# Kernel optimization log

Hardware: AMD Instinct MI355X
Metric: run time of the kernel (lower is better)

## Reference

```python
import jax, jax.numpy as jnp
import numpy as np

DIM = 128
HEADS = 4
WH, WW = 7, 7
N = WH * WW
NW = 256   # windows per image (mask groups)
B = 64     # batch images
B_ = NW * B


def _relative_position_index():
    coords = np.stack(np.meshgrid(np.arange(WH), np.arange(WW), indexing='ij'))  # [2,Wh,Ww]
    cf = coords.reshape(2, -1)
    rel = cf[:, :, None] - cf[:, None, :]          # [2,N,N]
    rel = rel.transpose(1, 2, 0).copy()
    rel[:, :, 0] += WH - 1
    rel[:, :, 1] += WW - 1
    rel[:, :, 0] *= 2 * WW - 1
    return rel.sum(-1).astype(np.int32)            # [N,N]


def setup_inputs() -> dict:
    key = jax.random.key(0)
    ks = jax.random.split(key, 8)
    std = 0.02
    return {
        'x': jax.random.normal(ks[0], (B_, N, DIM), jnp.float32),
        'mask': jax.random.normal(ks[1], (NW, N, N), jnp.float32),
        'qkv_w': jax.random.normal(ks[2], (3 * DIM, DIM), jnp.float32) * std,
        'qkv_b': jnp.zeros((3 * DIM,), jnp.float32),
        'proj_w': jax.random.normal(ks[3], (DIM, DIM), jnp.float32) * std,
        'proj_b': jnp.zeros((DIM,), jnp.float32),
        'rpb_table': jax.random.normal(ks[4], ((2 * WH - 1) * (2 * WW - 1), HEADS), jnp.float32) * std,
        'rpi': jnp.asarray(_relative_position_index()),
    }


def reference(x, mask, qkv_w, qkv_b, proj_w, proj_b, rpb_table, rpi):
    head_dim = DIM // HEADS
    scale = head_dim ** -0.5
    # qkv projection: [B_, N, 3*C] -> [3, B_, H, N, hd]
    qkv = (jnp.einsum('bnc,dc->bnd', x, qkv_w) + qkv_b)
    qkv = qkv.reshape(B_, N, 3, HEADS, head_dim).transpose(2, 0, 3, 1, 4)
    q, k, v = qkv[0] * scale, qkv[1], qkv[2]
    attn = jnp.einsum('bhnd,bhmd->bhnm', q, k)       # [B_, H, N, N]
    # gathered relative position bias: [N,N,H] -> [H,N,N]
    bias = rpb_table[rpi.reshape(-1)].reshape(N, N, HEADS).transpose(2, 0, 1)
    attn = attn + bias[None]
    # additive window mask: group B_ into (B, NW)
    attn = attn.reshape(B_ // NW, NW, HEADS, N, N) + mask[None, :, None]
    attn = attn.reshape(B_, HEADS, N, N)
    attn = jax.nn.softmax(attn, axis=-1)
    out = jnp.einsum('bhnm,bhmd->bnhd', attn, v).reshape(B_, N, DIM)
    out = jnp.einsum('bnc,dc->bnd', out, proj_w) + proj_b
    return out
```

## Files before the change

### kernel.cpp

```cpp
#include <hip/hip_runtime.h>

typedef __attribute__((ext_vector_type(8))) short sh8;
typedef __attribute__((ext_vector_type(4))) float f32x4;

#define MFMA(a, b, c) __builtin_amdgcn_mfma_f32_16x16x32_bf16(a, b, c, 0, 0, 0)

__device__ __forceinline__ short f2bf(float f) {
    unsigned u = __builtin_bit_cast(unsigned, f);
    u += 0x7fffu + ((u >> 16) & 1u);
    return (short)(u >> 16);
}

#define B_   16384
#define NW   256
#define NT   49
#define DIM  128
#define HEADS 4
#define HD   32
#define SCALE 0.17677669529663687f

#define V_BYTES     205520896u
#define AMASK_OFF   205520896u
#define QW_OFF      222298112u
#define PW_OFF      222396416u

__global__ __launch_bounds__(256) void wa_prep(
    const float* __restrict__ mask, const float* __restrict__ rpb,
    const int* __restrict__ rpi, const float* __restrict__ qkv_w,
    const float* __restrict__ proj_w, float* __restrict__ amask,
    short* __restrict__ qw, short* __restrict__ pw) {
    int g = blockIdx.x * 256 + threadIdx.x;
    int c = g & 63, r = (g >> 6) & 63, wi = (g >> 12) & 255, h = g >> 20;
    float v;
    if (c < NT) {
        v = 0.f;
        if (r < NT) {
            int idx = r * NT + c;
            v = rpb[rpi[idx] * HEADS + h] + mask[wi * (NT * NT) + idx];
        }
    } else {
        v = -1e30f;
    }
    amask[g] = v;
    if (g < 384 * 128) qw[g] = f2bf(qkv_w[g]);
    if (g < 128 * 128) pw[g] = f2bf(proj_w[g]);
}

__global__ __launch_bounds__(256, 2) void wa_qkv(
    const float* __restrict__ x, const short* __restrict__ qw,
    const float* __restrict__ qkv_b, short* __restrict__ qk,
    short* __restrict__ vbuf) {
    __shared__ short lA[128 * 152];
    __shared__ short lB[128 * 152];
    const int tid = threadIdx.x;
    const int bid = blockIdx.x;
    const int sel = bid % 3;
    const int bm  = bid / 3;

    {
        const float* xb = x + (size_t)bm * 128 * 128;
#pragma unroll
        for (int i = 0; i < 8; i++) {
            int chunk = i * 256 + tid;
            int row = chunk >> 4, col = (chunk & 15) * 8;
            float4 v0 = *(const float4*)(xb + row * 128 + col);
            float4 v1 = *(const float4*)(xb + row * 128 + col + 4);
            sh8 o;
            o[0] = f2bf(v0.x); o[1] = f2bf(v0.y); o[2] = f2bf(v0.z); o[3] = f2bf(v0.w);
            o[4] = f2bf(v1.x); o[5] = f2bf(v1.y); o[6] = f2bf(v1.z); o[7] = f2bf(v1.w);
            *(sh8*)(&lA[row * 152 + col]) = o;
        }
        const short* wb = qw + sel * 128 * 128;
#pragma unroll
        for (int i = 0; i < 8; i++) {
            int chunk = i * 256 + tid;
            int row = chunk >> 4, col = (chunk & 15) * 8;
            *(sh8*)(&lB[row * 152 + col]) = *(const sh8*)(wb + row * 128 + col);
        }
    }
    __syncthreads();

    const int lane = tid & 63, wid = tid >> 6;
    const int quad = lane >> 4, l15 = lane & 15;
    const int wm = (wid & 1) * 64, wn = (wid >> 1) * 64;

    f32x4 acc[4][4] = {};
#pragma unroll
    for (int ks = 0; ks < 4; ks++) {
        sh8 a[4], b[4];
#pragma unroll
        for (int t = 0; t < 4; t++)
            a[t] = *(const sh8*)(&lA[(wm + t * 16 + l15) * 152 + ks * 32 + quad * 8]);
#pragma unroll
        for (int t = 0; t < 4; t++)
            b[t] = *(const sh8*)(&lB[(wn + t * 16 + l15) * 152 + ks * 32 + quad * 8]);
#pragma unroll
        for (int ti = 0; ti < 4; ti++)
#pragma unroll
            for (int tj = 0; tj < 4; tj++)
                acc[ti][tj] = MFMA(a[ti], b[tj], acc[ti][tj]);
    }

    float bv[4]; int hh[4], ee[4];
#pragma unroll
    for (int tj = 0; tj < 4; tj++) {
        int n = wn + tj * 16 + l15;
        bv[tj] = qkv_b[sel * 128 + n];
        hh[tj] = n >> 5; ee[tj] = n & 31;
    }
    short* outp = (sel < 2) ? qk : vbuf;
#pragma unroll
    for (int ti = 0; ti < 4; ti++)
#pragma unroll
        for (int reg = 0; reg < 4; reg++) {
            int t = bm * 128 + wm + ti * 16 + quad * 4 + reg;
            unsigned bwin = (unsigned)t / 49u;
            int nn = t - bwin * 49u;
#pragma unroll
            for (int tj = 0; tj < 4; tj++) {
                float v = acc[ti][tj][reg] + bv[tj];
                if (sel == 0) v *= SCALE;
                size_t dst;
                if (sel < 2)
                    dst = (size_t)bwin * 12544 + (size_t)sel * 6272 +
                          (size_t)(hh[tj] * NT + nn) * HD + ee[tj];
                else
                    dst = (((size_t)bwin * HEADS + hh[tj]) * NT + nn) * HD + ee[tj];
                outp[dst] = f2bf(v);
            }
        }
}

__global__ __launch_bounds__(256, 2) void wa_attn(
    const short* __restrict__ qk, const short* __restrict__ vbuf,
    const float* __restrict__ amask, const short* __restrict__ pw,
    const float* __restrict__ proj_b, float* __restrict__ out) {
    __shared__ short smem[33792];
    const int tid = threadIdx.x, lane = tid & 63, wid = tid >> 6;
    const int quad = lane >> 4, l15 = lane & 15;
    const int b = blockIdx.x, wi = b & 255;
    short* Pl = smem + wid * 5632;
    short* Vl = smem + 22528 + wid * 2816;

    {
        const short* vb = vbuf + ((size_t)b * HEADS + wid) * NT * HD;
#pragma unroll
        for (int i = 0; i < 4; i++) {
            int chunk = i * 64 + lane;
            int token = chunk >> 2, colc = (chunk & 3) * 8;
            sh8 v = (sh8)(short)0;
            if (token < NT) v = *(const sh8*)(vb + token * HD + colc);
#pragma unroll
            for (int j = 0; j < 8; j++) Vl[(colc + j) * 88 + token] = v[j];
        }
    }

    const short* qb = qk + (size_t)b * 12544 + wid * NT * HD;
    const short* kb = qb + 6272;
    sh8 aq[4], bk[4];
#pragma unroll
    for (int t = 0; t < 4; t++) {
        int tok = t * 16 + l15;
        sh8 z = (sh8)(short)0;
        aq[t] = z; bk[t] = z;
        if (tok < NT) {
            aq[t] = *(const sh8*)(qb + tok * HD + quad * 8);
            bk[t] = *(const sh8*)(kb + tok * HD + quad * 8);
        }
    }
    f32x4 S[4][4] = {};
#pragma unroll
    for (int ti = 0; ti < 4; ti++)
#pragma unroll
        for (int tj = 0; tj < 4; tj++) S[ti][tj] = MFMA(aq[ti], bk[tj], S[ti][tj]);

    const float* am = amask + (((size_t)wid * NW + wi) << 12);
    float rinv[4][4];
#pragma unroll
    for (int ti = 0; ti < 4; ti++)
#pragma unroll
        for (int reg = 0; reg < 4; reg++) {
            int row = ti * 16 + quad * 4 + reg;
            float mx = -1e38f;
#pragma unroll
            for (int tj = 0; tj < 4; tj++) {
                float lg = S[ti][tj][reg] + am[row * 64 + tj * 16 + l15];
                S[ti][tj][reg] = lg;
                mx = fmaxf(mx, lg);
            }
#pragma unroll
            for (int d = 1; d < 16; d <<= 1) mx = fmaxf(mx, __shfl_xor(mx, d, 64));
            float sum = 0.f;
#pragma unroll
            for (int tj = 0; tj < 4; tj++) {
                float p = __expf(S[ti][tj][reg] - mx);
                S[ti][tj][reg] = p;
                sum += p;
            }
#pragma unroll
            for (int d = 1; d < 16; d <<= 1) sum += __shfl_xor(sum, d, 64);
            rinv[ti][reg] = 1.f / sum;
        }

#pragma unroll
    for (int ti = 0; ti < 4; ti++)
#pragma unroll
        for (int reg = 0; reg < 4; reg++) {
            int row = ti * 16 + quad * 4 + reg;
#pragma unroll
            for (int tj = 0; tj < 4; tj++)
                Pl[row * 88 + tj * 16 + l15] = f2bf(S[ti][tj][reg]);
        }

    f32x4 CV[4][2] = {};
#pragma unroll
    for (int ks = 0; ks < 2; ks++) {
        sh8 pa[4], vv[2];
#pragma unroll
        for (int t = 0; t < 4; t++)
            pa[t] = *(const sh8*)(&Pl[(t * 16 + l15) * 88 + ks * 32 + quad * 8]);
#pragma unroll
        for (int t = 0; t < 2; t++)
            vv[t] = *(const sh8*)(&Vl[(t * 16 + l15) * 88 + ks * 32 + quad * 8]);
#pragma unroll
        for (int ti = 0; ti < 4; ti++)
#pragma unroll
            for (int tj = 0; tj < 2; tj++) CV[ti][tj] = MFMA(pa[ti], vv[tj], CV[ti][tj]);
    }

    __syncthreads();

#pragma unroll
    for (int ti = 0; ti < 4; ti++)
#pragma unroll
        for (int reg = 0; reg < 4; reg++) {
            int row = ti * 16 + quad * 4 + reg;
            float inv = rinv[ti][reg];
#pragma unroll
            for (int tj = 0; tj < 2; tj++)
                smem[row * 152 + wid * 32 + tj * 16 + l15] = f2bf(CV[ti][tj][reg] * inv);
        }
    __syncthreads();

    f32x4 O[4][2] = {};
    const short* pwb = pw + (wid * 32) * 128;
#pragma unroll
    for (int ks = 0; ks < 4; ks++) {
        sh8 ca[4], wb2[2];
#pragma unroll
        for (int t = 0; t < 4; t++)
            ca[t] = *(const sh8*)(&smem[(t * 16 + l15) * 152 + ks * 32 + quad * 8]);
#pragma unroll
        for (int t = 0; t < 2; t++)
            wb2[t] = *(const sh8*)(pwb + (t * 16 + l15) * 128 + ks * 32 + quad * 8);
#pragma unroll
        for (int ti = 0; ti < 4; ti++)
#pragma unroll
            for (int tj = 0; tj < 2; tj++) O[ti][tj] = MFMA(ca[ti], wb2[tj], O[ti][tj]);
    }
    float pb[2];
#pragma unroll
    for (int t = 0; t < 2; t++) pb[t] = proj_b[wid * 32 + t * 16 + l15];
    float* ob = out + (size_t)b * NT * DIM;
#pragma unroll
    for (int ti = 0; ti < 4; ti++)
#pragma unroll
        for (int reg = 0; reg < 4; reg++) {
            int row = ti * 16 + quad * 4 + reg;
            if (row < NT) {
#pragma unroll
                for (int tj = 0; tj < 2; tj++)
                    ob[row * DIM + wid * 32 + tj * 16 + l15] = O[ti][tj][reg] + pb[tj];
            }
        }
}

extern "C" void kernel_launch(void* const* d_in, const int* in_sizes, int n_in,
                              void* d_out, int out_size, void* d_ws, size_t ws_size,
                              hipStream_t stream) {
    const float* x      = (const float*)d_in[0];
    const float* mask   = (const float*)d_in[1];
    const float* qkv_w  = (const float*)d_in[2];
    const float* qkv_b  = (const float*)d_in[3];
    const float* proj_w = (const float*)d_in[4];
    const float* proj_b = (const float*)d_in[5];
    const float* rpb    = (const float*)d_in[6];
    const int*   rpi    = (const int*)d_in[7];

    char* ws = (char*)d_ws;
    short* vbuf  = (short*)ws;
    float* amask = (float*)(ws + AMASK_OFF);
    short* qw    = (short*)(ws + QW_OFF);
    short* pw    = (short*)(ws + PW_OFF);
    short* qkbuf = (short*)d_out;
    float* out   = (float*)d_out;

    wa_prep<<<16384, 256, 0, stream>>>(mask, rpb, rpi, qkv_w, proj_w, amask, qw, pw);
    wa_qkv<<<6272 * 3, 256, 0, stream>>>(x, qw, qkv_b, qkbuf, vbuf);
    wa_attn<<<B_, 256, 0, stream>>>(qkbuf, vbuf, amask, pw, proj_b, out);
}
```

Before: 1.246 ms.

## Reuse converted x tile across Q/K/V, transpose scores, and swizzle LDS

The QKV kernel now converts each x tile to bf16 once and loops over the three weight slices, reading weights straight from global memory instead of staging them in LDS. This removes the threefold x reads and conversions and halves LDS use, which allows higher occupancy. The attention kernel computes S transposed so each lane holds a query row's keys, letting it use vectorized float4 mask loads and cut the row reductions to two shuffles. It also normalizes P before writing it, packs bf16 with v_cvt_pk_bf16_f32, and uses XOR-swizzled LDS layouts in place of padded ones, shrinking shared memory. The risks are extra latency from global weight loads and possible bank conflicts from the swizzle pattern.

```diff
diff --git a/kernel.cpp b/kernel.cpp
--- a/kernel.cpp
+++ b/kernel.cpp
@@ -9,6 +9,11 @@
     unsigned u = __builtin_bit_cast(unsigned, f);
     u += 0x7fffu + ((u >> 16) & 1u);
     return (short)(u >> 16);
+}
+__device__ __forceinline__ unsigned pk_bf16(float lo, float hi) {
+    unsigned r;
+    asm("v_cvt_pk_bf16_f32 %0, %1, %2" : "=v"(r) : "v"(lo), "v"(hi));
+    return r;
 }
 
 #define B_   16384
@@ -46,36 +51,25 @@
     if (g < 128 * 128) pw[g] = f2bf(proj_w[g]);
 }
 
-__global__ __launch_bounds__(256, 2) void wa_qkv(
+__global__ __launch_bounds__(256, 4) void wa_qkv(
     const float* __restrict__ x, const short* __restrict__ qw,
     const float* __restrict__ qkv_b, short* __restrict__ qk,
     short* __restrict__ vbuf) {
     __shared__ short lA[128 * 152];
-    __shared__ short lB[128 * 152];
     const int tid = threadIdx.x;
-    const int bid = blockIdx.x;
-    const int sel = bid % 3;
-    const int bm  = bid / 3;
-
+    const int bm = blockIdx.x;
     {
-        const float* xb = x + (size_t)bm * 128 * 128;
+        const float* xb = x + (size_t)bm * (128 * 128);
 #pragma unroll
         for (int i = 0; i < 8; i++) {
             int chunk = i * 256 + tid;
             int row = chunk >> 4, col = (chunk & 15) * 8;
             float4 v0 = *(const float4*)(xb + row * 128 + col);
             float4 v1 = *(const float4*)(xb + row * 128 + col + 4);
-            sh8 o;
-            o[0] = f2bf(v0.x); o[1] = f2bf(v0.y); o[2] = f2bf(v0.z); o[3] = f2bf(v0.w);
-            o[4] = f2bf(v1.x); o[5] = f2bf(v1.y); o[6] = f2bf(v1.z); o[7] = f2bf(v1.w);
-            *(sh8*)(&lA[row * 152 + col]) = o;
-        }
-        const short* wb = qw + sel * 128 * 128;
-#pragma unroll
-        for (int i = 0; i < 8; i++) {
-            int chunk = i * 256 + tid;
-            int row = chunk >> 4, col = (chunk & 15) * 8;
-            *(sh8*)(&lB[row * 152 + col]) = *(const sh8*)(wb + row * 128 + col);
+            uint4 u;
+            u.x = pk_bf16(v0.x, v0.y); u.y = pk_bf16(v0.z, v0.w);
+            u.z = pk_bf16(v1.x, v1.y); u.w = pk_bf16(v1.z, v1.w);
+            *(uint4*)(&lA[row * 152 + col]) = u;
         }
     }
     __syncthreads();
@@ -84,66 +78,70 @@
     const int quad = lane >> 4, l15 = lane & 15;
     const int wm = (wid & 1) * 64, wn = (wid >> 1) * 64;
 
-    f32x4 acc[4][4] = {};
-#pragma unroll
-    for (int ks = 0; ks < 4; ks++) {
-        sh8 a[4], b[4];
-#pragma unroll
-        for (int t = 0; t < 4; t++)
-            a[t] = *(const sh8*)(&lA[(wm + t * 16 + l15) * 152 + ks * 32 + quad * 8]);
-#pragma unroll
-        for (int t = 0; t < 4; t++)
-            b[t] = *(const sh8*)(&lB[(wn + t * 16 + l15) * 152 + ks * 32 + quad * 8]);
-#pragma unroll
-        for (int ti = 0; ti < 4; ti++)
-#pragma unroll
-            for (int tj = 0; tj < 4; tj++)
-                acc[ti][tj] = MFMA(a[ti], b[tj], acc[ti][tj]);
-    }
-
-    float bv[4]; int hh[4], ee[4];
-#pragma unroll
-    for (int tj = 0; tj < 4; tj++) {
-        int n = wn + tj * 16 + l15;
-        bv[tj] = qkv_b[sel * 128 + n];
-        hh[tj] = n >> 5; ee[tj] = n & 31;
-    }
-    short* outp = (sel < 2) ? qk : vbuf;
-#pragma unroll
-    for (int ti = 0; ti < 4; ti++)
-#pragma unroll
-        for (int reg = 0; reg < 4; reg++) {
-            int t = bm * 128 + wm + ti * 16 + quad * 4 + reg;
-            unsigned bwin = (unsigned)t / 49u;
-            int nn = t - bwin * 49u;
-#pragma unroll
-            for (int tj = 0; tj < 4; tj++) {
-                float v = acc[ti][tj][reg] + bv[tj];
-                if (sel == 0) v *= SCALE;
-                size_t dst;
-                if (sel < 2)
-                    dst = (size_t)bwin * 12544 + (size_t)sel * 6272 +
-                          (size_t)(hh[tj] * NT + nn) * HD + ee[tj];
-                else
-                    dst = (((size_t)bwin * HEADS + hh[tj]) * NT + nn) * HD + ee[tj];
-                outp[dst] = f2bf(v);
+#pragma unroll 1
+    for (int sel = 0; sel < 3; sel++) {
+        const short* wb = qw + sel * (128 * 128);
+        f32x4 acc[4][4] = {};
+#pragma unroll
+        for (int ks = 0; ks < 4; ks++) {
+            sh8 a[4], b[4];
+#pragma unroll
+            for (int t = 0; t < 4; t++)
+                a[t] = *(const sh8*)(&lA[(wm + t * 16 + l15) * 152 + ks * 32 + quad * 8]);
+#pragma unroll
+            for (int t = 0; t < 4; t++)
+                b[t] = *(const sh8*)(wb + (wn + t * 16 + l15) * 128 + ks * 32 + quad * 8);
+#pragma unroll
+            for (int ti = 0; ti < 4; ti++)
+#pragma unroll
+                for (int tj = 0; tj < 4; tj++)
+                    acc[ti][tj] = MFMA(a[ti], b[tj], acc[ti][tj]);
+        }
+        float bv[4]; int hh[4], ee[4];
+#pragma unroll
+        for (int tj = 0; tj < 4; tj++) {
+            int n = wn + tj * 16 + l15;
+            bv[tj] = qkv_b[sel * 128 + n];
+            hh[tj] = n >> 5; ee[tj] = n & 31;
+        }
+        short* outp = (sel < 2) ? qk : vbuf;
+#pragma unroll
+        for (int ti = 0; ti < 4; ti++)
+#pragma unroll
+            for (int reg = 0; reg < 4; reg++) {
+                int t = bm * 128 + wm + ti * 16 + quad * 4 + reg;
+                unsigned bwin = (unsigned)t / 49u;
+                int nn = t - bwin * 49u;
+#pragma unroll
+                for (int tj = 0; tj < 4; tj++) {
+                    float v = acc[ti][tj][reg] + bv[tj];
+                    if (sel == 0) v *= SCALE;
+                    size_t dst;
+                    if (sel < 2)
+                        dst = (size_t)bwin * 12544 + (size_t)sel * 6272 +
+                              (size_t)(hh[tj] * NT + nn) * HD + ee[tj];
+                    else
+                        dst = (((size_t)bwin * HEADS + hh[tj]) * NT + nn) * HD + ee[tj];
+                    outp[dst] = f2bf(v);
+                }
             }
-        }
-}
-
-__global__ __launch_bounds__(256, 2) void wa_attn(
+    }
+}
+
+__global__ __launch_bounds__(256, 3) void wa_attn(
     const short* __restrict__ qk, const short* __restrict__ vbuf,
     const float* __restrict__ amask, const short* __restrict__ pw,
     const float* __restrict__ proj_b, float* __restrict__ out) {
-    __shared__ short smem[33792];
+    __shared__ short smem[24576];
     const int tid = threadIdx.x, lane = tid & 63, wid = tid >> 6;
     const int quad = lane >> 4, l15 = lane & 15;
     const int b = blockIdx.x, wi = b & 255;
-    short* Pl = smem + wid * 5632;
-    short* Vl = smem + 22528 + wid * 2816;
+    short* Pl = smem + wid * 4096;
+    short* Vl = smem + 16384 + wid * 2048;
+    const int swz = (l15 & 7) << 3;
 
     {
-        const short* vb = vbuf + ((size_t)b * HEADS + wid) * NT * HD;
+        const short* vb = vbuf + ((size_t)b * HEADS + wid) * (NT * HD);
 #pragma unroll
         for (int i = 0; i < 4; i++) {
             int chunk = i * 64 + lane;
@@ -151,11 +149,12 @@
             sh8 v = (sh8)(short)0;
             if (token < NT) v = *(const sh8*)(vb + token * HD + colc);
 #pragma unroll
-            for (int j = 0; j < 8; j++) Vl[(colc + j) * 88 + token] = v[j];
-        }
-    }
-
-    const short* qb = qk + (size_t)b * 12544 + wid * NT * HD;
+            for (int j = 0; j < 8; j++)
+                Vl[(colc + j) * 64 + (token ^ (j << 3))] = v[j];
+        }
+    }
+
+    const short* qb = qk + (size_t)b * 12544 + wid * (NT * HD);
     const short* kb = qb + 6272;
     sh8 aq[4], bk[4];
 #pragma unroll
@@ -172,73 +171,72 @@
 #pragma unroll
     for (int ti = 0; ti < 4; ti++)
 #pragma unroll
-        for (int tj = 0; tj < 4; tj++) S[ti][tj] = MFMA(aq[ti], bk[tj], S[ti][tj]);
+        for (int tj = 0; tj < 4; tj++) S[ti][tj] = MFMA(bk[ti], aq[tj], S[ti][tj]);
 
     const float* am = amask + (((size_t)wid * NW + wi) << 12);
-    float rinv[4][4];
+#pragma unroll
+    for (int tj = 0; tj < 4; tj++) {
+        const int q = tj * 16 + l15;
+        float mx = -1e38f;
+#pragma unroll
+        for (int ti = 0; ti < 4; ti++) {
+            float4 m4 = *(const float4*)(am + q * 64 + ti * 16 + quad * 4);
+            S[ti][tj][0] += m4.x; S[ti][tj][1] += m4.y;
+            S[ti][tj][2] += m4.z; S[ti][tj][3] += m4.w;
+#pragma unroll
+            for (int r = 0; r < 4; r++) mx = fmaxf(mx, S[ti][tj][r]);
+        }
+        mx = fmaxf(mx, __shfl_xor(mx, 16));
+        mx = fmaxf(mx, __shfl_xor(mx, 32));
+        float sum = 0.f;
+#pragma unroll
+        for (int ti = 0; ti < 4; ti++)
+#pragma unroll
+            for (int r = 0; r < 4; r++) {
+                float p = __expf(S[ti][tj][r] - mx);
+                S[ti][tj][r] = p;
+                sum += p;
+            }
+        sum += __shfl_xor(sum, 16);
+        sum += __shfl_xor(sum, 32);
+        float inv = 1.f / sum;
+        short* pq = Pl + q * 64;
+#pragma unroll
+        for (int ti = 0; ti < 4; ti++) {
+            uint2 u;
+            u.x = pk_bf16(S[ti][tj][0] * inv, S[ti][tj][1] * inv);
+            u.y = pk_bf16(S[ti][tj][2] * inv, S[ti][tj][3] * inv);
+            *(uint2*)(pq + ((ti * 16 + quad * 4) ^ swz)) = u;
+        }
+    }
+
+    f32x4 CV[4][2] = {};
+#pragma unroll
+    for (int ks = 0; ks < 2; ks++) {
+        sh8 pa[4], vv[2];
+#pragma unroll
+        for (int t = 0; t < 4; t++)
+            pa[t] = *(const sh8*)(Pl + (t * 16 + l15) * 64 + ((ks * 32 + quad * 8) ^ swz));
+#pragma unroll
+        for (int t = 0; t < 2; t++)
+            vv[t] = *(const sh8*)(Vl + (t * 16 + l15) * 64 + ((ks * 32 + quad * 8) ^ swz));
+#pragma unroll
+        for (int ti = 0; ti < 4; ti++)
+#pragma unroll
+            for (int tj = 0; tj < 2; tj++) CV[ti][tj] = MFMA(pa[ti], vv[tj], CV[ti][tj]);
+    }
+
+    __syncthreads();
+
 #pragma unroll
     for (int ti = 0; ti < 4; ti++)
 #pragma unroll
         for (int reg = 0; reg < 4; reg++) {
             int row = ti * 16 + quad * 4 + reg;
-            float mx = -1e38f;
-#pragma unroll
-            for (int tj = 0; tj < 4; tj++) {
-                float lg = S[ti][tj][reg] + am[row * 64 + tj * 16 + l15];
-                S[ti][tj][reg] = lg;
-                mx = fmaxf(mx, lg);
-            }
-#pragma unroll
-            for (int d = 1; d < 16; d <<= 1) mx = fmaxf(mx, __shfl_xor(mx, d, 64));
-            float sum = 0.f;
-#pragma unroll
-            for (int tj = 0; tj < 4; tj++) {
-                float p = __expf(S[ti][tj][reg] - mx);
-                S[ti][tj][reg] = p;
-                sum += p;
-            }
-#pragma unroll
-            for (int d = 1; d < 16; d <<= 1) sum += __shfl_xor(sum, d, 64);
-            rinv[ti][reg] = 1.f / sum;
-        }
-
-#pragma unroll
-    for (int ti = 0; ti < 4; ti++)
-#pragma unroll
-        for (int reg = 0; reg < 4; reg++) {
-            int row = ti * 16 + quad * 4 + reg;
-#pragma unroll
-            for (int tj = 0; tj < 4; tj++)
-                Pl[row * 88 + tj * 16 + l15] = f2bf(S[ti][tj][reg]);
-        }
-
-    f32x4 CV[4][2] = {};
-#pragma unroll
-    for (int ks = 0; ks < 2; ks++) {
-        sh8 pa[4], vv[2];
-#pragma unroll
-        for (int t = 0; t < 4; t++)
-            pa[t] = *(const sh8*)(&Pl[(t * 16 + l15) * 88 + ks * 32 + quad * 8]);
-#pragma unroll
-        for (int t = 0; t < 2; t++)
-            vv[t] = *(const sh8*)(&Vl[(t * 16 + l15) * 88 + ks * 32 + quad * 8]);
-#pragma unroll
-        for (int ti = 0; ti < 4; ti++)
-#pragma unroll
-            for (int tj = 0; tj < 2; tj++) CV[ti][tj] = MFMA(pa[ti], vv[tj], CV[ti][tj]);
-    }
-
-    __syncthreads();
-
-#pragma unroll
-    for (int ti = 0; ti < 4; ti++)
-#pragma unroll
-        for (int reg = 0; reg < 4; reg++) {
-            int row = ti * 16 + quad * 4 + reg;
-            float inv = rinv[ti][reg];
+            int rs = (row & 7) << 3;
 #pragma unroll
             for (int tj = 0; tj < 2; tj++)
-                smem[row * 152 + wid * 32 + tj * 16 + l15] = f2bf(CV[ti][tj][reg] * inv);
+                smem[row * 128 + ((wid * 32 + tj * 16 + l15) ^ rs)] = f2bf(CV[ti][tj][reg]);
         }
     __syncthreads();
 
@@ -249,7 +247,7 @@
         sh8 ca[4], wb2[2];
 #pragma unroll
         for (int t = 0; t < 4; t++)
-            ca[t] = *(const sh8*)(&smem[(t * 16 + l15) * 152 + ks * 32 + quad * 8]);
+            ca[t] = *(const sh8*)(&smem[(t * 16 + l15) * 128 + ((ks * 32 + quad * 8) ^ swz)]);
 #pragma unroll
         for (int t = 0; t < 2; t++)
             wb2[t] = *(const sh8*)(pwb + (t * 16 + l15) * 128 + ks * 32 + quad * 8);
@@ -261,7 +259,7 @@
     float pb[2];
 #pragma unroll
     for (int t = 0; t < 2; t++) pb[t] = proj_b[wid * 32 + t * 16 + l15];
-    float* ob = out + (size_t)b * NT * DIM;
+    float* ob = out + (size_t)b * (NT * DIM);
 #pragma unroll
     for (int ti = 0; ti < 4; ti++)
 #pragma unroll
@@ -296,6 +294,6 @@
     float* out   = (float*)d_out;
 
     wa_prep<<<16384, 256, 0, stream>>>(mask, rpb, rpi, qkv_w, proj_w, amask, qw, pw);
-    wa_qkv<<<6272 * 3, 256, 0, stream>>>(x, qw, qkv_b, qkbuf, vbuf);
+    wa_qkv<<<6272, 256, 0, stream>>>(x, qw, qkv_b, qkbuf, vbuf);
     wa_attn<<<B_, 256, 0, stream>>>(qkbuf, vbuf, amask, pw, proj_b, out);
 }
```

New measurement: 3.045 ms. 144% more time.
